# Performance work log

Hardware: AMD Instinct MI355X
Metric: run time of the kernel (lower is better)

The kernel has to match this reference:

```python
import jax, jax.numpy as jnp
import numpy as np

D_MODEL = 1024
NUM_HEADS = 16
D_K = D_MODEL // NUM_HEADS
THETA = 10000.0
SEQ = 2048
BATCH = 2


def _rope(t, positions):
    # t: [b, h, s, d_k]; positions: [s]
    half = D_K // 2
    freqs = 1.0 / (THETA ** (jnp.arange(0, D_K, 2, dtype=jnp.float32) / D_K))  # [half]
    angles = positions.astype(jnp.float32)[:, None] * freqs[None, :]  # [s, half]
    cos = jnp.cos(angles)  # [s, half]
    sin = jnp.sin(angles)
    tr = t.reshape(t.shape[:-1] + (half, 2))  # pairs are (even, odd) interleaved
    x1, x2 = tr[..., 0], tr[..., 1]
    r1 = x1 * cos - x2 * sin
    r2 = x1 * sin + x2 * cos
    return jnp.stack([r1, r2], axis=-1).reshape(t.shape)


def setup_inputs() -> dict:
    key = jax.random.key(0)
    ks = jax.random.split(key, 5)
    std = float(np.sqrt(2.0 / (D_MODEL + D_MODEL)))
    return {
        "x": jax.random.normal(ks[0], (BATCH, SEQ, D_MODEL), dtype=jnp.float32),
        "token_positions": jnp.arange(SEQ, dtype=jnp.int64 if jax.config.jax_enable_x64 else jnp.int32),
        "wq": std * jax.random.normal(ks[1], (D_MODEL, D_MODEL), dtype=jnp.float32),
        "wk": std * jax.random.normal(ks[2], (D_MODEL, D_MODEL), dtype=jnp.float32),
        "wv": std * jax.random.normal(ks[3], (D_MODEL, D_MODEL), dtype=jnp.float32),
        "wo": std * jax.random.normal(ks[4], (D_MODEL, D_MODEL), dtype=jnp.float32),
    }


def reference(x, token_positions, wq, wk, wv, wo):
    b, s, _ = x.shape
    # projections: weight is (d_out, d_in), y = x @ W^T
    def proj(w):
        y = jnp.einsum('bsd,od->bso', x, w)
        return y.reshape(b, s, NUM_HEADS, D_K).transpose(0, 2, 1, 3)  # [b,h,s,dk]
    Q, K, V = proj(wq), proj(wk), proj(wv)
    Q = _rope(Q, token_positions)
    K = _rope(K, token_positions)
    scale = 1.0 / jnp.sqrt(jnp.asarray(D_K, dtype=x.dtype))
    scores = jnp.einsum('bhqd,bhkd->bhqk', Q, K) * scale  # [b,h,s,s]
    causal = jnp.tril(jnp.ones((s, s), dtype=bool))
    scores = jnp.where(causal, scores, jnp.asarray(-jnp.inf, dtype=scores.dtype))
    attn = jax.nn.softmax(scores, axis=-1)
    out = jnp.einsum('bhqk,bhkd->bhqd', attn, V)  # [b,h,s,dk]
    out = out.transpose(0, 2, 1, 3).reshape(b, s, D_MODEL)
    return jnp.einsum('bsd,od->bso', out, wo)
```

## Files before the change

kernel.cpp:

```cpp
#include <hip/hip_runtime.h>
#include <hip/hip_bf16.h>
#include <math.h>

#define BATCH  2
#define SEQ    2048
#define DMODEL 1024
#define NHEADS 16
#define DK     64

typedef __hip_bfloat16 bf16;
typedef short s16x8 __attribute__((ext_vector_type(8)));
typedef float f32x4 __attribute__((ext_vector_type(4)));

union P8 { int4 i4; s16x8 v; short s[8]; };

static __device__ __forceinline__ unsigned short f2bu(float f) {
    bf16 h = __float2bfloat16(f);
    return *reinterpret_cast<unsigned short*>(&h);
}
static __device__ __forceinline__ unsigned short f2bu_t(float f) {
    return (unsigned short)(__float_as_uint(f) >> 16);
}

static __device__ __forceinline__ void gll16(const void* g, void* l) {
    __builtin_amdgcn_global_load_lds(
        (const __attribute__((address_space(1))) unsigned int*)g,
        (__attribute__((address_space(3))) unsigned int*)l, 16, 0, 0);
}

__global__ __launch_bounds__(256) void conv_k(
    const float* __restrict__ x, const float* __restrict__ wq,
    const float* __restrict__ wk, const float* __restrict__ wv,
    const float* __restrict__ wo, bf16* __restrict__ dst)
{
    const size_t e0 = ((size_t)blockIdx.x * 256 + threadIdx.x) << 3;
    const float* src;
    bf16* d;
    if (e0 < (size_t)4194304) { src = x + e0; d = dst + e0; }
    else {
        const size_t r = e0 - 4194304;
        const int wsel = (int)(r >> 20);
        const size_t off = r & 1048575;
        src = (wsel == 0 ? wq : wsel == 1 ? wk : wsel == 2 ? wv : wo) + off;
        d = dst + 4194304 + ((size_t)wsel << 20) + off;
    }
    const float4 a = *(const float4*)src;
    const float4 b = *(const float4*)(src + 4);
    P8 p;
    p.s[0] = (short)f2bu(a.x); p.s[1] = (short)f2bu(a.y);
    p.s[2] = (short)f2bu(a.z); p.s[3] = (short)f2bu(a.w);
    p.s[4] = (short)f2bu(b.x); p.s[5] = (short)f2bu(b.y);
    p.s[6] = (short)f2bu(b.z); p.s[7] = (short)f2bu(b.w);
    *(int4*)d = p.i4;
}

__global__ __launch_bounds__(256) void gemm_qkv(
    const bf16* __restrict__ Ab, const bf16* __restrict__ Wb,
    bf16* __restrict__ O0, bf16* __restrict__ O1, bf16* __restrict__ O2)
{
    __shared__ __align__(16) short As[128 * 64];
    __shared__ __align__(16) short Ws[128 * 64];
    const int tid  = threadIdx.x;
    const int w    = tid >> 6;
    const int lane = tid & 63;
    const int ln   = lane & 15;
    const int quad = lane >> 4;
    const int id   = blockIdx.x;
    const int m_base = (id & 31) << 7;
    const int n_base = ((id >> 5) & 7) << 7;
    const int z = id >> 8;
    const bf16* Wz = Wb + ((size_t)z << 20);

    const int lrw = lane >> 3;
    const int lcs = ((lane & 7) ^ lrw) << 3;
    const size_t abase = (size_t)(m_base + 32 * w + lrw) * DMODEL + lcs;
    const size_t wbase = (size_t)(n_base + 32 * w + lrw) * DMODEL + lcs;
    short* ldsA = &As[2048 * w];
    short* ldsW = &Ws[2048 * w];

    const f32x4 zero4 = {0.f, 0.f, 0.f, 0.f};
    f32x4 acc[4][4];
    #pragma unroll
    for (int i = 0; i < 4; ++i)
        #pragma unroll
        for (int j = 0; j < 4; ++j) acc[i][j] = zero4;

    const int mo = (w >> 1) << 6, no = (w & 1) << 6;
    const int swz = ln & 7;

    for (int k0 = 0; k0 < DMODEL; k0 += 64) {
        __syncthreads();
        #pragma unroll
        for (int t = 0; t < 4; ++t) {
            gll16(Ab + abase + (size_t)t * 8 * DMODEL + k0, ldsA + t * 512);
            gll16(Wz + wbase + (size_t)t * 8 * DMODEL + k0, ldsW + t * 512);
        }
        __syncthreads();
        #pragma unroll
        for (int t = 0; t < 2; ++t) {
            const int co = (((t << 2) + quad) ^ swz) << 3;
            s16x8 af[4], bw[4];
            #pragma unroll
            for (int i = 0; i < 4; ++i) {
                af[i] = *(const s16x8*)&As[(mo + 16 * i + ln) * 64 + co];
                bw[i] = *(const s16x8*)&Ws[(no + 16 * i + ln) * 64 + co];
            }
            #pragma unroll
            for (int mi = 0; mi < 4; ++mi)
                #pragma unroll
                for (int ni = 0; ni < 4; ++ni)
                    acc[mi][ni] = __builtin_amdgcn_mfma_f32_16x16x32_bf16(
                        af[mi], bw[ni], acc[mi][ni], 0, 0, 0);
        }
    }

    if (z < 2) {
        bf16* C = (z == 0) ? O0 : O1;
        const float qs = (z == 0) ? 0.18033688011f : 1.0f;
        const int h = (n_base + no) >> 6;
        const float sgn = (ln & 1) ? 1.0f : -1.0f;
        float freq[4];
        #pragma unroll
        for (int ni = 0; ni < 4; ++ni)
            freq[ni] = exp2f(-(float)((16 * ni + ln) >> 1) * 0.4152410119f);
        #pragma unroll
        for (int mi = 0; mi < 4; ++mi) {
            #pragma unroll
            for (int r = 0; r < 4; ++r) {
                const int m = m_base + mo + 16 * mi + quad * 4 + r;
                const int b = m >> 11, s = m & (SEQ - 1);
                const float fs = (float)s;
                float sn[4], cs[4];
                #pragma unroll
                for (int ni = 0; ni < 4; ++ni)
                    __sincosf(fs * freq[ni], &sn[ni], &cs[ni]);
                bf16* row = C + (((size_t)(b * NHEADS + h) * SEQ) + s) * DK;
                #pragma unroll
                for (int ni = 0; ni < 4; ++ni) {
                    const float v = acc[mi][ni][r];
                    const float p = __shfl_xor(v, 1, 64);
                    row[16 * ni + ln] =
                        __float2bfloat16((v * cs[ni] + sgn * p * sn[ni]) * qs);
                }
            }
        }
    } else {
        #pragma unroll
        for (int ni = 0; ni < 4; ++ni) {
            const int n = n_base + no + 16 * ni + ln;
            const int h = n >> 6, d = n & (DK - 1);
            #pragma unroll
            for (int mi = 0; mi < 4; ++mi) {
                const int m0v = m_base + mo + 16 * mi + quad * 4;
                const int b = m0v >> 11, s0 = m0v & (SEQ - 1);
                ushort4 pk;
                pk.x = f2bu(acc[mi][ni][0]); pk.y = f2bu(acc[mi][ni][1]);
                pk.z = f2bu(acc[mi][ni][2]); pk.w = f2bu(acc[mi][ni][3]);
                *(ushort4*)(O2 + (((size_t)(b * NHEADS + h) * DK) + d) * SEQ + s0) = pk;
            }
        }
    }
}

__global__ __launch_bounds__(256) void gemm_wo(
    const bf16* __restrict__ Ab, const bf16* __restrict__ Wb,
    float* __restrict__ Of)
{
    __shared__ __align__(16) short As[64 * 64];
    __shared__ __align__(16) short Ws[128 * 64];
    const int tid  = threadIdx.x;
    const int w    = tid >> 6;
    const int lane = tid & 63;
    const int ln   = lane & 15;
    const int quad = lane >> 4;
    const int id   = blockIdx.x;
    const int m_base = (id & 63) << 6;
    const int n_base = (id >> 6) << 7;

    const int lrw = lane >> 3;
    const int lcs = ((lane & 7) ^ lrw) << 3;
    const int am = m_base + 16 * w + lrw;
    short* ldsA = &As[1024 * w];
    const size_t wbase = (size_t)(n_base + 32 * w + lrw) * DMODEL + lcs;
    short* ldsW = &Ws[2048 * w];

    const f32x4 zero4 = {0.f, 0.f, 0.f, 0.f};
    f32x4 acc[2][4];
    #pragma unroll
    for (int i = 0; i < 2; ++i)
        #pragma unroll
        for (int j = 0; j < 4; ++j) acc[i][j] = zero4;

    const int mo = (w >> 1) << 5, no = (w & 1) << 6;
    const int swz = ln & 7;

    for (int k0 = 0; k0 < DMODEL; k0 += 64) {
        const int hh = k0 >> 6;
        __syncthreads();
        #pragma unroll
        for (int t = 0; t < 2; ++t) {
            const int m = am + t * 8;
            const int b = m >> 11, s = m & (SEQ - 1);
            gll16(Ab + (((size_t)(b * NHEADS + hh) * SEQ) + s) * DK + lcs,
                  ldsA + t * 512);
        }
        #pragma unroll
        for (int t = 0; t < 4; ++t)
            gll16(Wb + wbase + (size_t)t * 8 * DMODEL + k0, ldsW + t * 512);
        __syncthreads();
        #pragma unroll
        for (int t = 0; t < 2; ++t) {
            const int co = (((t << 2) + quad) ^ swz) << 3;
            s16x8 af[2], bw[4];
            #pragma unroll
            for (int i = 0; i < 2; ++i)
                af[i] = *(const s16x8*)&As[(mo + 16 * i + ln) * 64 + co];
            #pragma unroll
            for (int j = 0; j < 4; ++j)
                bw[j] = *(const s16x8*)&Ws[(no + 16 * j + ln) * 64 + co];
            #pragma unroll
            for (int mi = 0; mi < 2; ++mi)
                #pragma unroll
                for (int ni = 0; ni < 4; ++ni)
                    acc[mi][ni] = __builtin_amdgcn_mfma_f32_16x16x32_bf16(
                        af[mi], bw[ni], acc[mi][ni], 0, 0, 0);
        }
    }

    #pragma unroll
    for (int mi = 0; mi < 2; ++mi)
        #pragma unroll
        for (int ni = 0; ni < 4; ++ni) {
            const int n = n_base + no + 16 * ni + ln;
            #pragma unroll
            for (int r = 0; r < 4; ++r) {
                const int m = m_base + mo + 16 * mi + quad * 4 + r;
                Of[(size_t)m * DMODEL + n] = acc[mi][ni][r];
            }
        }
}

__global__ __launch_bounds__(256) void attn_k(bf16* __restrict__ Q,
                                              const bf16* __restrict__ Kg,
                                              const bf16* __restrict__ VT)
{
    __shared__ __align__(16) short Ks[2][64 * 72];
    __shared__ __align__(16) short Vs[2][64 * 72];
    __shared__ __align__(16) short PT[64 * 72];
    const int tid  = threadIdx.x;
    const int w    = tid >> 6;
    const int lane = tid & 63;
    const int ln   = lane & 15;
    const int quad = lane >> 4;
    const int bh = blockIdx.x & 31;
    const int qt = 31 - (blockIdx.x >> 5);
    const size_t base = (size_t)bh * (SEQ * DK);
    const int srow = tid >> 2;
    const int sc   = (tid & 3) << 4;
    const int qrow = qt * 64 + 16 * w + ln;

    P8 qa0, qa1;
    {
        const bf16* qsrc = Q + base + (size_t)qrow * DK + quad * 8;
        qa0.i4 = *(const int4*)(qsrc);
        qa1.i4 = *(const int4*)(qsrc + 32);
    }
    const f32x4 zero4 = {0.f, 0.f, 0.f, 0.f};
    f32x4 o[4];
    #pragma unroll
    for (int mt = 0; mt < 4; ++mt) o[mt] = zero4;
    float lsum = 0.f;

    P8 kk[2], vv[2];
    {
        const bf16* ksrc = Kg + base + (size_t)srow * DK + sc;
        kk[0].i4 = *(const int4*)(ksrc);
        kk[1].i4 = *(const int4*)(ksrc + 8);
        const bf16* vsrc = VT + base + (size_t)srow * SEQ + sc;
        vv[0].i4 = *(const int4*)(vsrc);
        vv[1].i4 = *(const int4*)(vsrc + 8);
    }

    for (int kb = 0; kb <= qt; ++kb) {
        const int pb = kb & 1;
        *(s16x8*)&Ks[pb][srow * 72 + sc]     = kk[0].v;
        *(s16x8*)&Ks[pb][srow * 72 + sc + 8] = kk[1].v;
        *(s16x8*)&Vs[pb][srow * 72 + sc]     = vv[0].v;
        *(s16x8*)&Vs[pb][srow * 72 + sc + 8] = vv[1].v;
        __syncthreads();

        if (kb < qt) {
            const bf16* ksrc = Kg + base + (size_t)((kb + 1) * 64 + srow) * DK + sc;
            kk[0].i4 = *(const int4*)(ksrc);
            kk[1].i4 = *(const int4*)(ksrc + 8);
            const bf16* vsrc = VT + base + (size_t)srow * SEQ + (kb + 1) * 64 + sc;
            vv[0].i4 = *(const int4*)(vsrc);
            vv[1].i4 = *(const int4*)(vsrc + 8);
        }

        f32x4 sf[4];
        #pragma unroll
        for (int mt = 0; mt < 4; ++mt) {
            sf[mt] = zero4;
            s16x8 ka  = *(const s16x8*)&Ks[pb][(16 * mt + ln) * 72 + quad * 8];
            s16x8 kb2 = *(const s16x8*)&Ks[pb][(16 * mt + ln) * 72 + 32 + quad * 8];
            sf[mt] = __builtin_amdgcn_mfma_f32_16x16x32_bf16(ka,  qa0.v, sf[mt], 0, 0, 0);
            sf[mt] = __builtin_amdgcn_mfma_f32_16x16x32_bf16(kb2, qa1.v, sf[mt], 0, 0, 0);
        }

        if (kb == qt) {
            #pragma unroll
            for (int mt = 0; mt < 4; ++mt)
                #pragma unroll
                for (int r = 0; r < 4; ++r)
                    if (kb * 64 + 16 * mt + quad * 4 + r > qrow) sf[mt][r] = -INFINITY;
        }
        #pragma unroll
        for (int mt = 0; mt < 4; ++mt)
            #pragma unroll
            for (int r = 0; r < 4; ++r) {
                sf[mt][r] = exp2f(sf[mt][r]);
                lsum += sf[mt][r];
            }

        #pragma unroll
        for (int mt = 0; mt < 4; ++mt) {
            ushort4 pk;
            pk.x = f2bu_t(sf[mt][0]); pk.y = f2bu_t(sf[mt][1]);
            pk.z = f2bu_t(sf[mt][2]); pk.w = f2bu_t(sf[mt][3]);
            *(ushort4*)&PT[(16 * w + ln) * 72 + 16 * mt + quad * 4] = pk;
        }

        s16x8 pa0 = *(const s16x8*)&PT[(16 * w + ln) * 72 + quad * 8];
        s16x8 pa1 = *(const s16x8*)&PT[(16 * w + ln) * 72 + 32 + quad * 8];
        #pragma unroll
        for (int mt = 0; mt < 4; ++mt) {
            s16x8 va0 = *(const s16x8*)&Vs[pb][(16 * mt + ln) * 72 + quad * 8];
            s16x8 va1 = *(const s16x8*)&Vs[pb][(16 * mt + ln) * 72 + 32 + quad * 8];
            o[mt] = __builtin_amdgcn_mfma_f32_16x16x32_bf16(va0, pa0, o[mt], 0, 0, 0);
            o[mt] = __builtin_amdgcn_mfma_f32_16x16x32_bf16(va1, pa1, o[mt], 0, 0, 0);
        }
    }

    lsum += __shfl_xor(lsum, 16, 64);
    lsum += __shfl_xor(lsum, 32, 64);
    const float inv = 1.0f / lsum;
    #pragma unroll
    for (int mt = 0; mt < 4; ++mt) {
        ushort4 st;
        st.x = f2bu(o[mt][0] * inv); st.y = f2bu(o[mt][1] * inv);
        st.z = f2bu(o[mt][2] * inv); st.w = f2bu(o[mt][3] * inv);
        *(ushort4*)(Q + base + (size_t)qrow * DK + 16 * mt + quad * 4) = st;
    }
}

extern "C" void kernel_launch(void* const* d_in, const int* in_sizes, int n_in,
                              void* d_out, int out_size, void* d_ws, size_t ws_size,
                              hipStream_t stream)
{
    const float* x  = (const float*)d_in[0];
    const float* wq = (const float*)d_in[2];
    const float* wk = (const float*)d_in[3];
    const float* wv = (const float*)d_in[4];
    const float* wo = (const float*)d_in[5];

    bf16* wsb   = (bf16*)d_ws;
    bf16* xb    = wsb;
    bf16* wqkvb = wsb + ((size_t)4 << 20);
    bf16* wob   = wsb + ((size_t)7 << 20);
    bf16* Qw    = wsb + ((size_t)8 << 20);
    bf16* Kw    = wsb + ((size_t)12 << 20);
    bf16* VTw   = wsb + ((size_t)16 << 20);

    conv_k<<<4096, 256, 0, stream>>>(x, wq, wk, wv, wo, wsb);
    gemm_qkv<<<768, 256, 0, stream>>>(xb, wqkvb, Qw, Kw, VTw);
    attn_k<<<1024, 256, 0, stream>>>(Qw, Kw, VTw);
    gemm_wo<<<512, 256, 0, stream>>>(Qw, wob, (float*)d_out);
}
```

Before: 177.6 us.

## Software-pipeline attention loop: defer PV MFMA one iteration, triple-buffer V

```diff
diff --git a/kernel.cpp b/kernel.cpp
--- a/kernel.cpp
+++ b/kernel.cpp
@@ -18,8 +18,8 @@
     bf16 h = __float2bfloat16(f);
     return *reinterpret_cast<unsigned short*>(&h);
 }
-static __device__ __forceinline__ unsigned short f2bu_t(float f) {
-    return (unsigned short)(__float_as_uint(f) >> 16);
+static __device__ __forceinline__ unsigned int pk2(float a, float b) {
+    return __builtin_amdgcn_perm(__float_as_uint(b), __float_as_uint(a), 0x07060302u);
 }
 
 static __device__ __forceinline__ void gll16(const void* g, void* l) {
@@ -153,10 +153,10 @@
             for (int mi = 0; mi < 4; ++mi) {
                 const int m0v = m_base + mo + 16 * mi + quad * 4;
                 const int b = m0v >> 11, s0 = m0v & (SEQ - 1);
-                ushort4 pk;
-                pk.x = f2bu(acc[mi][ni][0]); pk.y = f2bu(acc[mi][ni][1]);
-                pk.z = f2bu(acc[mi][ni][2]); pk.w = f2bu(acc[mi][ni][3]);
-                *(ushort4*)(O2 + (((size_t)(b * NHEADS + h) * DK) + d) * SEQ + s0) = pk;
+                ushort4 pkv;
+                pkv.x = f2bu(acc[mi][ni][0]); pkv.y = f2bu(acc[mi][ni][1]);
+                pkv.z = f2bu(acc[mi][ni][2]); pkv.w = f2bu(acc[mi][ni][3]);
+                *(ushort4*)(O2 + (((size_t)(b * NHEADS + h) * DK) + d) * SEQ + s0) = pkv;
             }
         }
     }
@@ -240,13 +240,14 @@
         }
 }
 
+#define STR 68
 __global__ __launch_bounds__(256) void attn_k(bf16* __restrict__ Q,
                                               const bf16* __restrict__ Kg,
                                               const bf16* __restrict__ VT)
 {
-    __shared__ __align__(16) short Ks[2][64 * 72];
-    __shared__ __align__(16) short Vs[2][64 * 72];
-    __shared__ __align__(16) short PT[64 * 72];
+    __shared__ __align__(16) short Ks[2][64 * STR];
+    __shared__ __align__(16) short Vs[3][64 * STR];
+    __shared__ __align__(16) short PT[64 * STR];
     const int tid  = threadIdx.x;
     const int w    = tid >> 6;
     const int lane = tid & 63;
@@ -280,32 +281,63 @@
         vv[0].i4 = *(const int4*)(vsrc);
         vv[1].i4 = *(const int4*)(vsrc + 8);
     }
+    *(s16x8*)&Ks[0][srow * STR + sc]     = kk[0].v;
+    *(s16x8*)&Ks[0][srow * STR + sc + 8] = kk[1].v;
+    *(s16x8*)&Vs[0][srow * STR + sc]     = vv[0].v;
+    *(s16x8*)&Vs[0][srow * STR + sc + 8] = vv[1].v;
+    if (qt > 0) {
+        const bf16* ksrc = Kg + base + (size_t)(64 + srow) * DK + sc;
+        kk[0].i4 = *(const int4*)(ksrc);
+        kk[1].i4 = *(const int4*)(ksrc + 8);
+        const bf16* vsrc = VT + base + (size_t)srow * SEQ + 64 + sc;
+        vv[0].i4 = *(const int4*)(vsrc);
+        vv[1].i4 = *(const int4*)(vsrc + 8);
+    }
+
+    const int prow = (16 * w + ln) * STR;
 
     for (int kb = 0; kb <= qt; ++kb) {
-        const int pb = kb & 1;
-        *(s16x8*)&Ks[pb][srow * 72 + sc]     = kk[0].v;
-        *(s16x8*)&Ks[pb][srow * 72 + sc + 8] = kk[1].v;
-        *(s16x8*)&Vs[pb][srow * 72 + sc]     = vv[0].v;
-        *(s16x8*)&Vs[pb][srow * 72 + sc + 8] = vv[1].v;
         __syncthreads();
 
-        if (kb < qt) {
-            const bf16* ksrc = Kg + base + (size_t)((kb + 1) * 64 + srow) * DK + sc;
-            kk[0].i4 = *(const int4*)(ksrc);
-            kk[1].i4 = *(const int4*)(ksrc + 8);
-            const bf16* vsrc = VT + base + (size_t)srow * SEQ + (kb + 1) * 64 + sc;
-            vv[0].i4 = *(const int4*)(vsrc);
-            vv[1].i4 = *(const int4*)(vsrc + 8);
-        }
-
+        const short* Kb = Ks[kb & 1];
         f32x4 sf[4];
         #pragma unroll
         for (int mt = 0; mt < 4; ++mt) {
             sf[mt] = zero4;
-            s16x8 ka  = *(const s16x8*)&Ks[pb][(16 * mt + ln) * 72 + quad * 8];
-            s16x8 kb2 = *(const s16x8*)&Ks[pb][(16 * mt + ln) * 72 + 32 + quad * 8];
+            s16x8 ka  = *(const s16x8*)&Kb[(16 * mt + ln) * STR + quad * 8];
+            s16x8 kb2 = *(const s16x8*)&Kb[(16 * mt + ln) * STR + 32 + quad * 8];
             sf[mt] = __builtin_amdgcn_mfma_f32_16x16x32_bf16(ka,  qa0.v, sf[mt], 0, 0, 0);
             sf[mt] = __builtin_amdgcn_mfma_f32_16x16x32_bf16(kb2, qa1.v, sf[mt], 0, 0, 0);
+        }
+
+        if (kb > 0) {
+            const short* Vb = Vs[(kb - 1) % 3];
+            s16x8 pa0 = *(const s16x8*)&PT[prow + quad * 8];
+            s16x8 pa1 = *(const s16x8*)&PT[prow + 32 + quad * 8];
+            #pragma unroll
+            for (int mt = 0; mt < 4; ++mt) {
+                s16x8 va0 = *(const s16x8*)&Vb[(16 * mt + ln) * STR + quad * 8];
+                s16x8 va1 = *(const s16x8*)&Vb[(16 * mt + ln) * STR + 32 + quad * 8];
+                o[mt] = __builtin_amdgcn_mfma_f32_16x16x32_bf16(va0, pa0, o[mt], 0, 0, 0);
+                o[mt] = __builtin_amdgcn_mfma_f32_16x16x32_bf16(va1, pa1, o[mt], 0, 0, 0);
+            }
+        }
+
+        if (kb < qt) {
+            const int nb = (kb + 1) & 1;
+            const int nv = (kb + 1) % 3;
+            *(s16x8*)&Ks[nb][srow * STR + sc]     = kk[0].v;
+            *(s16x8*)&Ks[nb][srow * STR + sc + 8] = kk[1].v;
+            *(s16x8*)&Vs[nv][srow * STR + sc]     = vv[0].v;
+            *(s16x8*)&Vs[nv][srow * STR + sc + 8] = vv[1].v;
+            if (kb + 1 < qt) {
+                const bf16* ksrc = Kg + base + (size_t)((kb + 2) * 64 + srow) * DK + sc;
+                kk[0].i4 = *(const int4*)(ksrc);
+                kk[1].i4 = *(const int4*)(ksrc + 8);
+                const bf16* vsrc = VT + base + (size_t)srow * SEQ + (kb + 2) * 64 + sc;
+                vv[0].i4 = *(const int4*)(vsrc);
+                vv[1].i4 = *(const int4*)(vsrc + 8);
+            }
         }
 
         if (kb == qt) {
@@ -322,21 +354,23 @@
                 sf[mt][r] = exp2f(sf[mt][r]);
                 lsum += sf[mt][r];
             }
-
         #pragma unroll
         for (int mt = 0; mt < 4; ++mt) {
-            ushort4 pk;
-            pk.x = f2bu_t(sf[mt][0]); pk.y = f2bu_t(sf[mt][1]);
-            pk.z = f2bu_t(sf[mt][2]); pk.w = f2bu_t(sf[mt][3]);
-            *(ushort4*)&PT[(16 * w + ln) * 72 + 16 * mt + quad * 4] = pk;
-        }
-
-        s16x8 pa0 = *(const s16x8*)&PT[(16 * w + ln) * 72 + quad * 8];
-        s16x8 pa1 = *(const s16x8*)&PT[(16 * w + ln) * 72 + 32 + quad * 8];
+            uint2 pw;
+            pw.x = pk2(sf[mt][0], sf[mt][1]);
+            pw.y = pk2(sf[mt][2], sf[mt][3]);
+            *(uint2*)&PT[prow + 16 * mt + quad * 4] = pw;
+        }
+    }
+
+    {
+        const short* Vb = Vs[qt % 3];
+        s16x8 pa0 = *(const s16x8*)&PT[prow + quad * 8];
+        s16x8 pa1 = *(const s16x8*)&PT[prow + 32 + quad * 8];
         #pragma unroll
         for (int mt = 0; mt < 4; ++mt) {
-            s16x8 va0 = *(const s16x8*)&Vs[pb][(16 * mt + ln) * 72 + quad * 8];
-            s16x8 va1 = *(const s16x8*)&Vs[pb][(16 * mt + ln) * 72 + 32 + quad * 8];
+            s16x8 va0 = *(const s16x8*)&Vb[(16 * mt + ln) * STR + quad * 8];
+            s16x8 va1 = *(const s16x8*)&Vb[(16 * mt + ln) * STR + 32 + quad * 8];
             o[mt] = __builtin_amdgcn_mfma_f32_16x16x32_bf16(va0, pa0, o[mt], 0, 0, 0);
             o[mt] = __builtin_amdgcn_mfma_f32_16x16x32_bf16(va1, pa1, o[mt], 0, 0, 0);
         }
```

New measurement: 279.1 us. 57.1% more time.
